# Kernel tuning notes

Measured on AMD Instinct MI355X. Metric: run time of the kernel, lower is better.

The kernel has to match this reference:

```python
import jax, jax.numpy as jnp
import numpy as np

E = 400000   # n_entity
R = 500      # n_relation
D = 128      # embed_dim
B = 2048     # batch of queries
K = 128      # sample_limit (refer neighbors per query)
GAMMA = 24.0
EPS = 2.0


def _xavier(key, fan_out, fan_in):
    lim = np.sqrt(6.0 / (fan_in + fan_out)).astype(np.float32)
    return jax.random.uniform(key, (fan_out, fan_in), minval=-lim, maxval=lim, dtype=jnp.float32)


def setup_inputs() -> dict:
    key = jax.random.key(0)
    ks = jax.random.split(key, 9)
    erange = (GAMMA + EPS) / D
    # tables with the appended zero padding row (as in forward's torch.cat)
    ent = jax.random.uniform(ks[0], (E + R + 1, D), minval=-erange, maxval=erange, dtype=jnp.float32)
    entity_embedding = jnp.concatenate([ent, jnp.zeros((1, D), jnp.float32)], axis=0)
    rel = jax.random.uniform(ks[1], (R + 1, D), minval=-erange, maxval=erange, dtype=jnp.float32)
    relation_embedding = jnp.concatenate([rel, jnp.zeros((1, D), jnp.float32)], axis=0)
    off = jax.random.uniform(ks[2], (R + 1, D), minval=0.0, maxval=erange, dtype=jnp.float32)
    offset_embedding = jnp.concatenate([off, jnp.zeros((1, D), jnp.float32)], axis=0)
    # ProjectionAggregating attention MLP params
    W1 = _xavier(ks[3], D, 2 * D)
    b1 = jnp.zeros((D,), jnp.float32)
    W2 = _xavier(ks[4], D, D)
    b2 = jnp.zeros((D,), jnp.float32)
    anchors = jax.random.randint(ks[5], (B,), 0, E)
    rel_0 = jax.random.randint(ks[6], (B,), 0, R)
    p1_target = jax.random.randint(ks[7], (B, K), 0, E)
    p1_rel = jax.random.randint(ks[8], (B, K), 0, R)
    return {
        'entity_embedding': entity_embedding,
        'relation_embedding': relation_embedding,
        'offset_embedding': offset_embedding,
        'W1': W1, 'b1': b1, 'W2': W2, 'b2': b2,
        'anchors': anchors, 'rel_0': rel_0,
        'p1_target': p1_target, 'p1_rel': p1_rel,
    }


def reference(entity_embedding, relation_embedding, offset_embedding,
              W1, b1, W2, b2, anchors, rel_0, p1_target, p1_rel):
    # ---- '1p' query path of IDN_Q2B_24.forward ----
    h_a = entity_embedding[anchors]            # [B, D]
    r_q = relation_embedding[rel_0]            # [B, D]
    query_emb = h_a + r_q                      # [B, D]
    offset_emb = offset_embedding[rel_0]       # [B, D]  (activation = Identity)
    h_t = entity_embedding[p1_target]          # [B, K, D]  refer_embs
    r_t = relation_embedding[p1_rel]           # [B, K, D]  refer_r
    # ProjectionAggregating (aggr='bias'): bias = refer - (start + refer_r)
    bias = h_t - (h_a[:, None, :] + r_t)       # [B, K, D]
    x = jnp.concatenate([r_t, jnp.broadcast_to(r_q[:, None, :], r_t.shape)], axis=-1)  # [B,K,2D]
    a1 = jax.nn.relu(jnp.einsum('bkf,df->bkd', x, W1) + b1)   # [B, K, D]
    attn = jnp.einsum('bkd,ed->bke', a1, W2) + b2             # [B, K, D]
    final_refer = jnp.sum(attn * bias, axis=-2)               # [B, D]
    final_query = query_emb + final_refer
    return final_query, offset_emb
```

## Files before the change

### kernel.cpp

```cpp
#include <hip/hip_runtime.h>

typedef __attribute__((ext_vector_type(8))) short short8;
typedef __attribute__((ext_vector_type(4))) float f32x4;

#define NRELROWS 502
#define NB 2048
#define DD 128
#define OUT_HALF (NB * DD)

__device__ __forceinline__ short f2bf(float x) {
    union { float f; unsigned u; } c; c.f = x;
    return (short)((c.u + 0x7FFFu + ((c.u >> 16) & 1u)) >> 16);
}

__global__ __launch_bounds__(256) void precompute_kernel(
    const float* __restrict__ rel, const float* __restrict__ W1,
    const float* __restrict__ b1, const float* __restrict__ W2,
    float* __restrict__ U, float* __restrict__ V,
    unsigned short* __restrict__ W2f)
{
    const int bid = blockIdx.x;
    const int tid = threadIdx.x;
    if (bid < NRELROWS) {
        __shared__ float srel[DD];
        if (tid < DD) srel[tid] = rel[bid * DD + tid];
        __syncthreads();
        const int half = tid >> 7;
        const int d = tid & 127;
        const float* wrow = W1 + d * 256 + half * 128;
        float acc = 0.f;
#pragma unroll 8
        for (int f = 0; f < 128; f += 4) {
            float4 wv = *(const float4*)(wrow + f);
            acc += srel[f] * wv.x + srel[f + 1] * wv.y +
                   srel[f + 2] * wv.z + srel[f + 3] * wv.w;
        }
        if (half) {
            V[bid * DD + d] = acc + b1[d];
        } else {
            U[bid * DD + d] = acc;
        }
    } else {
        const int tile = bid - NRELROWS;
        const int kt = tile >> 3, nt = tile & 7;
#pragma unroll
        for (int e = 0; e < 2; ++e) {
            const int within = tid * 2 + e;
            const int l = within >> 3, i = within & 7;
            const int n = nt * 16 + (l & 15);
            const int f = kt * 32 + (l >> 4) * 8 + i;
            W2f[tile * 512 + within] = (unsigned short)f2bf(W2[n * 128 + f]);
        }
    }
}

__global__ __launch_bounds__(256) void main_kernel(
    const float* __restrict__ ent, const float* __restrict__ rel,
    const float* __restrict__ off, const float* __restrict__ b2,
    const int* __restrict__ anchors, const int* __restrict__ rel0,
    const int* __restrict__ p1t, const int* __restrict__ p1r,
    const float* __restrict__ U, const float* __restrict__ V,
    const unsigned short* __restrict__ W2f, float* __restrict__ out)
{
    const int b = blockIdx.x;
    const int tid = threadIdx.x;
    const int w = tid >> 6;
    const int l = tid & 63;
    const int lg = l >> 4;
    const int l15 = l & 15;

    const int aidx = anchors[b];
    const int r0 = rel0[b];
    const int* p1t_b = p1t + (b << 7);
    const int* p1r_b = p1r + (b << 7);

    int relA[2];
    relA[0] = p1r_b[(w << 5) + l15];
    relA[1] = p1r_b[(w << 5) + 16 + l15];

    f32x4 acc[2][8];
#pragma unroll
    for (int t = 0; t < 2; ++t)
#pragma unroll
        for (int n = 0; n < 8; ++n) acc[t][n] = (f32x4)0.f;

    const float* Vrow = V + r0 * DD;

#pragma unroll
    for (int kt = 0; kt < 4; ++kt) {
        const int f0 = kt * 32 + lg * 8;
        const float4 vv0 = *(const float4*)(Vrow + f0);
        const float4 vv1 = *(const float4*)(Vrow + f0 + 4);
        short8 af[2];
#pragma unroll
        for (int t = 0; t < 2; ++t) {
            const float* Urow = U + relA[t] * DD + f0;
            const float4 u0 = *(const float4*)(Urow);
            const float4 u1 = *(const float4*)(Urow + 4);
            af[t][0] = f2bf(fmaxf(u0.x + vv0.x, 0.f));
            af[t][1] = f2bf(fmaxf(u0.y + vv0.y, 0.f));
            af[t][2] = f2bf(fmaxf(u0.z + vv0.z, 0.f));
            af[t][3] = f2bf(fmaxf(u0.w + vv0.w, 0.f));
            af[t][4] = f2bf(fmaxf(u1.x + vv1.x, 0.f));
            af[t][5] = f2bf(fmaxf(u1.y + vv1.y, 0.f));
            af[t][6] = f2bf(fmaxf(u1.z + vv1.z, 0.f));
            af[t][7] = f2bf(fmaxf(u1.w + vv1.w, 0.f));
        }
        const unsigned short* Wk = W2f + (kt << 3) * 512 + (l << 3);
#pragma unroll
        for (int nt = 0; nt < 8; ++nt) {
            const short8 bf = *(const short8*)(Wk + (nt << 9));
            acc[0][nt] = __builtin_amdgcn_mfma_f32_16x16x32_bf16(af[0], bf, acc[0][nt], 0, 0, 0);
            acc[1][nt] = __builtin_amdgcn_mfma_f32_16x16x32_bf16(af[1], bf, acc[1][nt], 0, 0, 0);
        }
    }

    __shared__ float red[4][DD];
    int tg[2][4], rr[2][4];
#pragma unroll
    for (int t = 0; t < 2; ++t) {
        const int4 t4 = *(const int4*)(p1t_b + (w << 5) + (t << 4) + (lg << 2));
        const int4 r4 = *(const int4*)(p1r_b + (w << 5) + (t << 4) + (lg << 2));
        tg[t][0] = t4.x; tg[t][1] = t4.y; tg[t][2] = t4.z; tg[t][3] = t4.w;
        rr[t][0] = r4.x; rr[t][1] = r4.y; rr[t][2] = r4.z; rr[t][3] = r4.w;
    }
    const float* arow = ent + (size_t)aidx * DD;
#pragma unroll
    for (int nt = 0; nt < 8; ++nt) {
        const int d = (nt << 4) + l15;
        const float had = arow[d];
        const float b2d = b2[d];
        float ps = 0.f;
#pragma unroll
        for (int t = 0; t < 2; ++t) {
#pragma unroll
            for (int r2 = 0; r2 < 4; ++r2) {
                const float at = acc[t][nt][r2] + b2d;
                const float ht = ent[(size_t)tg[t][r2] * DD + d];
                const float rt = rel[rr[t][r2] * DD + d];
                ps += at * (ht - had - rt);
            }
        }
        ps += __shfl_xor(ps, 16);
        ps += __shfl_xor(ps, 32);
        if (lg == 0) red[w][d] = ps;
    }
    __syncthreads();
    if (tid < DD) {
        const int d = tid;
        const float s = red[0][d] + red[1][d] + red[2][d] + red[3][d];
        out[(b << 7) + d] = arow[d] + rel[r0 * DD + d] + s;
        out[OUT_HALF + (b << 7) + d] = off[r0 * DD + d];
    }
}

extern "C" void kernel_launch(void* const* d_in, const int* in_sizes, int n_in,
                              void* d_out, int out_size, void* d_ws, size_t ws_size,
                              hipStream_t stream) {
    const float* ent  = (const float*)d_in[0];
    const float* rel  = (const float*)d_in[1];
    const float* off  = (const float*)d_in[2];
    const float* W1   = (const float*)d_in[3];
    const float* b1   = (const float*)d_in[4];
    const float* W2   = (const float*)d_in[5];
    const float* b2   = (const float*)d_in[6];
    const int* anchors = (const int*)d_in[7];
    const int* rel0    = (const int*)d_in[8];
    const int* p1t     = (const int*)d_in[9];
    const int* p1r     = (const int*)d_in[10];
    float* out = (float*)d_out;

    float* U = (float*)d_ws;
    float* V = U + NRELROWS * DD;
    unsigned short* W2f = (unsigned short*)(V + NRELROWS * DD);

    precompute_kernel<<<NRELROWS + 32, 256, 0, stream>>>(rel, W1, b1, W2, U, V, W2f);
    main_kernel<<<NB, 256, 0, stream>>>(ent, rel, off, b2, anchors, rel0,
                                        p1t, p1r, U, V, W2f, out);
}
```

Before: 63.46 us.

## Prefetch neighbor entity rows into LDS asynchronously and batch relation rows in precompute

In the main kernel, each wave now issues direct global-to-LDS loads for its 32 gathered entity rows at kernel start, so the scattered gathers overlap with the MFMA attention computation instead of being issued as scalar loads afterward. The bias step then reads entity rows from LDS. The reduction buffer reuses that LDS area behind an extra barrier. Separately, the precompute kernel handles four relation rows per block, reusing each W1 load across four rows and cutting the block count. The cost is 64KB of LDS per block, which limits occupancy.

```diff
diff --git a/kernel.cpp b/kernel.cpp
--- a/kernel.cpp
+++ b/kernel.cpp
@@ -21,27 +21,38 @@
 {
     const int bid = blockIdx.x;
     const int tid = threadIdx.x;
-    if (bid < NRELROWS) {
-        __shared__ float srel[DD];
-        if (tid < DD) srel[tid] = rel[bid * DD + tid];
+    if (bid < 126) {
+        __shared__ float srel[4][DD];
+        const int r0 = bid << 2;
+        for (int i = tid; i < 512; i += 256) {
+            const int r = i >> 7, c = i & 127;
+            const int rr = r0 + r;
+            srel[r][c] = (rr < NRELROWS) ? rel[rr * DD + c] : 0.f;
+        }
         __syncthreads();
         const int half = tid >> 7;
         const int d = tid & 127;
         const float* wrow = W1 + d * 256 + half * 128;
-        float acc = 0.f;
+        float a0 = 0.f, a1 = 0.f, a2 = 0.f, a3 = 0.f;
 #pragma unroll 8
         for (int f = 0; f < 128; f += 4) {
-            float4 wv = *(const float4*)(wrow + f);
-            acc += srel[f] * wv.x + srel[f + 1] * wv.y +
-                   srel[f + 2] * wv.z + srel[f + 3] * wv.w;
-        }
-        if (half) {
-            V[bid * DD + d] = acc + b1[d];
-        } else {
-            U[bid * DD + d] = acc;
+            const float4 wv = *(const float4*)(wrow + f);
+            a0 += srel[0][f]*wv.x + srel[0][f+1]*wv.y + srel[0][f+2]*wv.z + srel[0][f+3]*wv.w;
+            a1 += srel[1][f]*wv.x + srel[1][f+1]*wv.y + srel[1][f+2]*wv.z + srel[1][f+3]*wv.w;
+            a2 += srel[2][f]*wv.x + srel[2][f+1]*wv.y + srel[2][f+2]*wv.z + srel[2][f+3]*wv.w;
+            a3 += srel[3][f]*wv.x + srel[3][f+1]*wv.y + srel[3][f+2]*wv.z + srel[3][f+3]*wv.w;
+        }
+        float res[4] = {a0, a1, a2, a3};
+        const float bb = half ? b1[d] : 0.f;
+#pragma unroll
+        for (int r = 0; r < 4; ++r) {
+            if (r0 + r < NRELROWS) {
+                if (half) V[(r0 + r) * DD + d] = res[r] + bb;
+                else      U[(r0 + r) * DD + d] = res[r];
+            }
         }
     } else {
-        const int tile = bid - NRELROWS;
+        const int tile = bid - 126;
         const int kt = tile >> 3, nt = tile & 7;
 #pragma unroll
         for (int e = 0; e < 2; ++e) {
@@ -62,17 +73,32 @@
     const float* __restrict__ U, const float* __restrict__ V,
     const unsigned short* __restrict__ W2f, float* __restrict__ out)
 {
+    __shared__ float ht[4][32][DD];
     const int b = blockIdx.x;
     const int tid = threadIdx.x;
     const int w = tid >> 6;
     const int l = tid & 63;
     const int lg = l >> 4;
     const int l15 = l & 15;
+    const int half = l >> 5;
 
     const int aidx = anchors[b];
     const int r0 = rel0[b];
     const int* p1t_b = p1t + (b << 7);
     const int* p1r_b = p1r + (b << 7);
+
+    int rowi[16];
+#pragma unroll
+    for (int j = 0; j < 16; ++j)
+        rowi[j] = p1t_b[(w << 5) + (j << 1) + half];
+#pragma unroll
+    for (int j = 0; j < 16; ++j) {
+        const float* g = ent + (size_t)rowi[j] * DD + ((l & 31) << 2);
+        float* lp = &ht[w][j << 1][0];
+        __builtin_amdgcn_global_load_lds(
+            (const __attribute__((address_space(1))) unsigned int*)g,
+            (__attribute__((address_space(3))) unsigned int*)lp, 16, 0, 0);
+    }
 
     int relA[2];
     relA[0] = p1r_b[(w << 5) + l15];
@@ -115,40 +141,50 @@
         }
     }
 
-    __shared__ float red[4][DD];
-    int tg[2][4], rr[2][4];
+    int rr[2][4];
 #pragma unroll
     for (int t = 0; t < 2; ++t) {
-        const int4 t4 = *(const int4*)(p1t_b + (w << 5) + (t << 4) + (lg << 2));
         const int4 r4 = *(const int4*)(p1r_b + (w << 5) + (t << 4) + (lg << 2));
-        tg[t][0] = t4.x; tg[t][1] = t4.y; tg[t][2] = t4.z; tg[t][3] = t4.w;
         rr[t][0] = r4.x; rr[t][1] = r4.y; rr[t][2] = r4.z; rr[t][3] = r4.w;
     }
     const float* arow = ent + (size_t)aidx * DD;
+
+    asm volatile("s_waitcnt vmcnt(0)" ::: "memory");
+    __builtin_amdgcn_sched_barrier(0);
+
+    float ps[8];
+#pragma unroll
+    for (int nt = 0; nt < 8; ++nt) ps[nt] = 0.f;
 #pragma unroll
     for (int nt = 0; nt < 8; ++nt) {
         const int d = (nt << 4) + l15;
         const float had = arow[d];
         const float b2d = b2[d];
-        float ps = 0.f;
 #pragma unroll
         for (int t = 0; t < 2; ++t) {
 #pragma unroll
             for (int r2 = 0; r2 < 4; ++r2) {
                 const float at = acc[t][nt][r2] + b2d;
-                const float ht = ent[(size_t)tg[t][r2] * DD + d];
-                const float rt = rel[rr[t][r2] * DD + d];
-                ps += at * (ht - had - rt);
+                const float htv = ht[w][(t << 4) + (lg << 2) + r2][d];
+                const float rtv = rel[rr[t][r2] * DD + d];
+                ps[nt] += at * (htv - had - rtv);
             }
         }
-        ps += __shfl_xor(ps, 16);
-        ps += __shfl_xor(ps, 32);
-        if (lg == 0) red[w][d] = ps;
+        ps[nt] += __shfl_xor(ps[nt], 16);
+        ps[nt] += __shfl_xor(ps[nt], 32);
+    }
+
+    __syncthreads();
+    float* red = &ht[0][0][0];
+    if (lg == 0) {
+#pragma unroll
+        for (int nt = 0; nt < 8; ++nt)
+            red[w * DD + (nt << 4) + l15] = ps[nt];
     }
     __syncthreads();
     if (tid < DD) {
         const int d = tid;
-        const float s = red[0][d] + red[1][d] + red[2][d] + red[3][d];
+        const float s = red[d] + red[DD + d] + red[2 * DD + d] + red[3 * DD + d];
         out[(b << 7) + d] = arow[d] + rel[r0 * DD + d] + s;
         out[OUT_HALF + (b << 7) + d] = off[r0 * DD + d];
     }
@@ -174,7 +210,7 @@
     float* V = U + NRELROWS * DD;
     unsigned short* W2f = (unsigned short*)(V + NRELROWS * DD);
 
-    precompute_kernel<<<NRELROWS + 32, 256, 0, stream>>>(rel, W1, b1, W2, U, V, W2f);
+    precompute_kernel<<<126 + 32, 256, 0, stream>>>(rel, W1, b1, W2, U, V, W2f);
     main_kernel<<<NB, 256, 0, stream>>>(ent, rel, off, b2, anchors, rel0,
                                         p1t, p1r, U, V, W2f, out);
 }
```

Result: faster. 56.68 us (-10.7%).
